# Optimization experiments

Hardware: AMD Instinct MI355X
Metric: run time of the kernel (lower is better)

## Reference

```python
import jax, jax.numpy as jnp
import numpy as np

EMB = 768
HEADS = 12
HEAD_DIM = EMB // HEADS
LN_EPS = 1e-5


def _layernorm(x, g, b):
    mu = jnp.mean(x, axis=-1, keepdims=True)
    var = jnp.mean(jnp.square(x - mu), axis=-1, keepdims=True)
    return (x - mu) * jax.lax.rsqrt(var + LN_EPS) * g + b


def _att_block(x, ln_g, ln_b, w_qkv, b_qkv, w_proj, b_proj):
    # x: [b, n, e]
    B, N, E = x.shape
    h, d = HEADS, HEAD_DIM
    qkv = _layernorm(x, ln_g, ln_b) @ w_qkv.T + b_qkv          # [b, n, 3e]
    # einops 'b n (h d qkv)': last axis factors as (h, d, 3), qkv innermost
    qkv = qkv.reshape(B, N, h, d, 3)
    qkv = jnp.moveaxis(qkv, (4, 2), (0, 2))                    # [3, b, h, n, d]
    q, k, v = qkv[0], qkv[1], qkv[2]
    scale = d ** (-0.5)
    # NOTE: original code DIVIDES by scale (= multiplies by sqrt(d)) -- faithful
    scores = jnp.einsum('bhqd,bhkd->bhqk', q, k) / scale       # [b, h, n, n]
    attn = jax.nn.softmax(scores, axis=-1)
    out = jnp.einsum('bhqk,bhkd->bhqd', attn, v)               # [b, h, n, d]
    out = out.transpose(0, 2, 1, 3).reshape(B, N, E)           # [b, n, e]
    return x + out @ w_proj.T + b_proj


def setup_inputs() -> dict:
    key = jax.random.key(0)
    ks = jax.random.split(key, 8)
    B, N, E = 2, 2048, EMB
    s = E ** (-0.5)
    return {
        'modal1': jax.random.normal(ks[0], (B, N, E), jnp.float32),
        'modal2': jax.random.normal(ks[1], (B, N, E), jnp.float32),
        'ln1_g': jnp.ones((E,), jnp.float32),
        'ln1_b': jnp.zeros((E,), jnp.float32),
        'w_qkv1': jax.random.normal(ks[2], (3 * E, E), jnp.float32) * s,
        'b_qkv1': jnp.zeros((3 * E,), jnp.float32),
        'w_proj1': jax.random.normal(ks[3], (E, E), jnp.float32) * s,
        'b_proj1': jnp.zeros((E,), jnp.float32),
        'ln2_g': jnp.ones((E,), jnp.float32),
        'ln2_b': jnp.zeros((E,), jnp.float32),
        'w_qkv2': jax.random.normal(ks[4], (3 * E, E), jnp.float32) * s,
        'b_qkv2': jnp.zeros((3 * E,), jnp.float32),
        'w_proj2': jax.random.normal(ks[5], (E, E), jnp.float32) * s,
        'b_proj2': jnp.zeros((E,), jnp.float32),
    }


def reference(modal1, modal2, ln1_g, ln1_b, w_qkv1, b_qkv1, w_proj1, b_proj1,
              ln2_g, ln2_b, w_qkv2, b_qkv2, w_proj2, b_proj2):
    out1 = _att_block(modal1, ln1_g, ln1_b, w_qkv1, b_qkv1, w_proj1, b_proj1)
    out2 = _att_block(modal2, ln2_g, ln2_b, w_qkv2, b_qkv2, w_proj2, b_proj2)
    return (out1, out2)
```

## Files before the change

kernel.cpp:

```cpp
#include <hip/hip_runtime.h>
#include <hip/hip_bf16.h>


typedef unsigned short u16;
typedef unsigned int   u32;
typedef __attribute__((ext_vector_type(4)))  float floatx4;
typedef __attribute__((ext_vector_type(16))) float floatx16;
typedef __attribute__((ext_vector_type(8)))  short shortx8;
typedef __attribute__((ext_vector_type(2)))  unsigned int uintx2;

#define EMB   768
#define SEQ   2048
#define NHEAD 12
#define HDIM  64
#define RPM   4096
#define NROW  8192
#define NUNIT 48
#define KTS   4096

__device__ __forceinline__ float bf2f(u16 h) {
  union { u32 u; float f; } v; v.u = ((u32)h) << 16; return v.f;
}
__device__ __forceinline__ u16 f2bf(float f) {
  union { float f; u32 u; } v; v.f = f;
  u32 r = v.u + 0x7fffu + ((v.u >> 16) & 1u);
  return (u16)(r >> 16);
}
__device__ __forceinline__ u32 cvtpk_bf16(float a, float b) {
  u32 r;
  asm("v_cvt_pk_bf16_f32 %0, %1, %2" : "=v"(r) : "v"(a), "v"(b));
  return r;
}
__device__ __forceinline__ void swap_halves(u32 a, u32 b, u32& x, u32& y) {
#if __has_builtin(__builtin_amdgcn_permlane32_swap)
  uintx2 r = __builtin_amdgcn_permlane32_swap(a, b, false, false);
  x = r.x; y = r.y;
#else
  u32 ax = (u32)__shfl_xor((int)a, 32);
  u32 bx = (u32)__shfl_xor((int)b, 32);
  bool h = (threadIdx.x & 32) != 0;
  x = h ? bx : a;
  y = h ? b : ax;
#endif
}

__global__ __launch_bounds__(256) void prep_wq(
    const float* __restrict__ wq1, const float* __restrict__ wq2,
    u16* __restrict__ wh, u16* __restrict__ wl)
{
  int bx = blockIdx.x;
  int modal = bx / 2304, rowp = bx % 2304;
  int typ = rowp / 768, hd = rowp % 768;
  const float* W = (modal ? wq2 : wq1) + (size_t)(hd * 3 + typ) * EMB;
  size_t dst = (size_t)bx * EMB;
  int t = threadIdx.x;
  #pragma unroll
  for (int i = 0; i < 3; ++i) {
    int e = t + i * 256;
    float v = W[e];
    u16 h = f2bf(v);
    wh[dst + e] = h;
    wl[dst + e] = f2bf(v - bf2f(h));
  }
}

__global__ __launch_bounds__(256) void prep_wp(
    const float* __restrict__ wp1, const float* __restrict__ wp2,
    u16* __restrict__ wh)
{
  int bx = blockIdx.x;
  int modal = bx / 768, row = bx % 768;
  const float* W = (modal ? wp2 : wp1) + (size_t)row * EMB;
  size_t dst = (size_t)bx * EMB;
  int t = threadIdx.x;
  #pragma unroll
  for (int i = 0; i < 3; ++i) {
    int e = t + i * 256;
    wh[dst + e] = f2bf(W[e]);
  }
}

__global__ __launch_bounds__(256) void k_ln(
    const float* __restrict__ x1, const float* __restrict__ x2,
    const float* __restrict__ g1, const float* __restrict__ b1,
    const float* __restrict__ g2, const float* __restrict__ b2,
    u16* __restrict__ xn_hi, u16* __restrict__ xn_lo)
{
  int row = blockIdx.x;
  int modal = row >> 12;
  const float* x = modal ? x2 : x1;
  const float* g = modal ? g2 : g1;
  const float* bb = modal ? b2 : b1;
  int r = row & (RPM - 1);
  const float* xr = x + (size_t)r * EMB;
  int t = threadIdx.x;
  float v0 = xr[t], v1 = xr[t + 256], v2 = xr[t + 512];
  float s = v0 + v1 + v2;
  float s2 = v0 * v0 + v1 * v1 + v2 * v2;
  #pragma unroll
  for (int m = 1; m < 64; m <<= 1) { s += __shfl_xor(s, m); s2 += __shfl_xor(s2, m); }
  __shared__ float ls[4], ls2[4];
  int w = t >> 6;
  if ((t & 63) == 0) { ls[w] = s; ls2[w] = s2; }
  __syncthreads();
  s = ls[0] + ls[1] + ls[2] + ls[3];
  s2 = ls2[0] + ls2[1] + ls2[2] + ls2[3];
  float mu = s * (1.0f / EMB);
  float var = s2 * (1.0f / EMB) - mu * mu;
  float rs = rsqrtf(var + 1e-5f);
  size_t base = (size_t)row * EMB;
  float vv[3] = { v0, v1, v2 };
  #pragma unroll
  for (int i = 0; i < 3; ++i) {
    int e = t + i * 256;
    float xn = (vv[i] - mu) * rs * g[e] + bb[e];
    u16 h = f2bf(xn);
    xn_hi[base + e] = h;
    xn_lo[base + e] = f2bf(xn - bf2f(h));
  }
}

__global__ __launch_bounds__(256) void k_qkv(
    const u16* __restrict__ xn_hi, const u16* __restrict__ xn_lo,
    const u16* __restrict__ wqh, const u16* __restrict__ wql,
    const float* __restrict__ bq1, const float* __restrict__ bq2,
    u16* __restrict__ q_hi, u16* __restrict__ q_lo,
    u16* __restrict__ k_hi, u16* __restrict__ k_lo,
    u16* __restrict__ vT)
{
  int mt = blockIdx.x, ntile = blockIdx.y, modal = blockIdx.z;
  const float* BQ = modal ? bq2 : bq1;
  int typ = ntile / 6;
  int hd0 = (ntile % 6) * 128;

  __shared__ __align__(16) u16 As_hi[2][128 * 32], Wh[2][128 * 32],
                               As_lo[2][128 * 32], Wl[2][128 * 32];

  int tid = threadIdx.x, lane = tid & 63, w = tid >> 6;
  int wm = (w >> 1) * 64, wn = (w & 1) * 64;
  int lc = lane & 15, lq = lane >> 4;

  int srow = lane >> 2;
  int schunk = ((lane & 3) ^ (srow & 3)) << 3;

  floatx4 acc[4][4] = {};
  const u16* aH = xn_hi + (size_t)(modal * RPM + mt * 128) * EMB;
  const u16* aL = xn_lo + (size_t)(modal * RPM + mt * 128) * EMB;
  const u16* wH = wqh + (size_t)(modal * 2304 + typ * 768 + hd0) * EMB;
  const u16* wL = wql + (size_t)(modal * 2304 + typ * 768 + hd0) * EMB;

  auto stage = [&](int buf, int k0) {
    if (typ != 2) {
      #pragma unroll
      for (int c = 0; c < 8; ++c) {
        int seg = w * 8 + c;
        int tile = seg >> 3, segin = seg & 7;
        size_t off = (size_t)(segin * 16 + srow) * EMB + k0 + schunk;
        const u16* src; u16* dstb;
        if (tile == 0)      { src = aH + off; dstb = &As_hi[buf][0]; }
        else if (tile == 1) { src = wH + off; dstb = &Wh[buf][0]; }
        else if (tile == 2) { src = aL + off; dstb = &As_lo[buf][0]; }
        else                { src = wL + off; dstb = &Wl[buf][0]; }
        __builtin_amdgcn_global_load_lds(
            (const __attribute__((address_space(1))) unsigned int*)src,
            (__attribute__((address_space(3))) unsigned int*)(dstb + segin * 512), 16, 0, 0);
      }
    } else {
      #pragma unroll
      for (int c = 0; c < 4; ++c) {
        int seg = w * 4 + c;
        int tile = seg >> 3, segin = seg & 7;
        size_t off = (size_t)(segin * 16 + srow) * EMB + k0 + schunk;
        const u16* src; u16* dstb;
        if (tile == 0) { src = aH + off; dstb = &As_hi[buf][0]; }
        else           { src = wH + off; dstb = &Wh[buf][0]; }
        __builtin_amdgcn_global_load_lds(
            (const __attribute__((address_space(1))) unsigned int*)src,
            (__attribute__((address_space(3))) unsigned int*)(dstb + segin * 512), 16, 0, 0);
      }
    }
  };

  stage(0, 0);
  for (int kk = 0; kk < 24; ++kk) {
    int cur = kk & 1;
    bool more = (kk + 1 < 24);
    if (more) stage(cur ^ 1, (kk + 1) * 32);
    if (typ != 2) {
      if (more) asm volatile("s_waitcnt vmcnt(8)" ::: "memory");
      else      asm volatile("s_waitcnt vmcnt(0)" ::: "memory");
    } else {
      if (more) asm volatile("s_waitcnt vmcnt(4)" ::: "memory");
      else      asm volatile("s_waitcnt vmcnt(0)" ::: "memory");
    }
    __builtin_amdgcn_s_barrier();
    __builtin_amdgcn_sched_barrier(0);

    shortx8 ah[4], al[4], whf[4], wlf[4];
    int rsw = lc & 3;
    int ca = (lq ^ rsw) << 3;
    #pragma unroll
    for (int i = 0; i < 4; ++i) {
      int ra = wm + i * 16 + lc, rw = wn + i * 16 + lc;
      ah[i]  = *(const shortx8*)&As_hi[cur][ra * 32 + ca];
      whf[i] = *(const shortx8*)&Wh[cur][rw * 32 + ca];
      if (typ != 2) {
        al[i]  = *(const shortx8*)&As_lo[cur][ra * 32 + ca];
        wlf[i] = *(const shortx8*)&Wl[cur][rw * 32 + ca];
      }
    }
    #pragma unroll
    for (int i = 0; i < 4; ++i)
      #pragma unroll
      for (int jn = 0; jn < 4; ++jn) {
        acc[i][jn] = __builtin_amdgcn_mfma_f32_16x16x32_bf16(ah[i], whf[jn], acc[i][jn], 0, 0, 0);
        if (typ != 2) {
          acc[i][jn] = __builtin_amdgcn_mfma_f32_16x16x32_bf16(al[i], whf[jn], acc[i][jn], 0, 0, 0);
          acc[i][jn] = __builtin_amdgcn_mfma_f32_16x16x32_bf16(ah[i], wlf[jn], acc[i][jn], 0, 0, 0);
        }
      }
    asm volatile("s_waitcnt lgkmcnt(0)" ::: "memory");
    __builtin_amdgcn_s_barrier();
    __builtin_amdgcn_sched_barrier(0);
  }

  #pragma unroll
  for (int i = 0; i < 4; ++i) {
    int mrow0 = mt * 128 + wm + i * 16 + lq * 4;
    #pragma unroll
    for (int jn = 0; jn < 4; ++jn) {
      int colp = hd0 + wn + jn * 16 + lc;
      int h = colp >> 6, d = colp & 63;
      float bias = BQ[colp * 3 + typ];
      #pragma unroll
      for (int r = 0; r < 4; ++r) {
        int mrow = mrow0 + r;
        int b = mrow >> 11, nq = mrow & (SEQ - 1);
        int uu = modal * 24 + b * 12 + h;
        float val = acc[i][jn][r] + bias;
        if (typ == 0) {
          size_t o = ((size_t)uu * SEQ + nq) * HDIM + d;
          u16 hh = f2bf(val); q_hi[o] = hh; q_lo[o] = f2bf(val - bf2f(hh));
        } else if (typ == 1) {
          size_t o = ((size_t)uu * SEQ + nq) * HDIM + d;
          u16 hh = f2bf(val); k_hi[o] = hh; k_lo[o] = f2bf(val - bf2f(hh));
        } else {
          vT[((size_t)uu * HDIM + d) * SEQ + nq] = f2bf(val);
        }
      }
    }
  }
}

__global__ __launch_bounds__(256, 3) void k_attn(
    const u16* __restrict__ q_hi, const u16* __restrict__ q_lo,
    const u16* __restrict__ k_hi, const u16* __restrict__ k_lo,
    const u16* __restrict__ vT, u16* __restrict__ attn_out)
{
  int id = blockIdx.x + (blockIdx.y << 4);
  int xcd = id & 7, j = id >> 3;
  int u = xcd * 6 + (j >> 4);
  int qt = j & 15;

  __shared__ __align__(16) u16 lds[2][3 * KTS];

  int tid = threadIdx.x, lane = tid & 63, w = tid >> 6;
  int col = lane & 31, hi = lane >> 5;
  int swz = (col & 7) << 4;

  shortx8 qh[4], qlo[4];
  {
    size_t qb = ((size_t)u * SEQ + qt * 128 + w * 32 + col) * HDIM + hi * 8;
    #pragma unroll
    for (int s = 0; s < 4; ++s) {
      qh[s]  = *(const shortx8*)(q_hi + qb + s * 16);
      qlo[s] = *(const shortx8*)(q_lo + qb + s * 16);
    }
  }

  int lrow = lane >> 3;
  int lcol = ((lane & 7) ^ lrow) << 3;
  const u16* kh_src = k_hi + (size_t)u * SEQ * HDIM;
  const u16* kl_src = k_lo + (size_t)u * SEQ * HDIM;
  const u16* v_src  = vT  + (size_t)u * HDIM * SEQ;

  auto stage = [&](int buf, int kc) {
    #pragma unroll
    for (int c = 0; c < 6; ++c) {
      int seg = w * 6 + c;
      int tile = seg >> 3, segin = seg & 7;
      u16* dst = &lds[buf][tile * KTS + segin * 512];
      const u16* src;
      if (tile == 0)      src = kh_src + (size_t)(kc + segin * 8 + lrow) * HDIM + lcol;
      else if (tile == 1) src = kl_src + (size_t)(kc + segin * 8 + lrow) * HDIM + lcol;
      else                src = v_src  + (size_t)(segin * 8 + lrow) * SEQ + kc + lcol;
      __builtin_amdgcn_global_load_lds(
          (const __attribute__((address_space(1))) unsigned int*)src,
          (__attribute__((address_space(3))) unsigned int*)dst, 16, 0, 0);
    }
  };

  shortx8 ONES;
  #pragma unroll
  for (int i = 0; i < 8; ++i) ONES[i] = (short)0x3F80;

  floatx16 O0 = {}, O1 = {};
  floatx16 Osum = {};
  float m_r = -1e30f;
  const float Cs = 11.5415603271f;
  const float THR = 8.0f;

  stage(0, 0);
  __syncthreads();

  for (int t = 0; t < SEQ / 64; ++t) {
    int cur = t & 1;
    if (t + 1 < SEQ / 64) stage(cur ^ 1, (t + 1) * 64);

    const char* Kh = (const char*)&lds[cur][0];
    const char* Kl = (const char*)&lds[cur][KTS];
    const char* Vt = (const char*)&lds[cur][2 * KTS];

    floatx16 S0 = {}, S1 = {};
    __builtin_amdgcn_s_setprio(1);
    #pragma unroll
    for (int s = 0; s < 4; ++s) {
      int cb = (s * 32 + hi * 16) ^ swz;
      shortx8 kf0 = *(const shortx8*)(Kh + col * 128 + cb);
      shortx8 kl0 = *(const shortx8*)(Kl + col * 128 + cb);
      shortx8 kf1 = *(const shortx8*)(Kh + (32 + col) * 128 + cb);
      shortx8 kl1 = *(const shortx8*)(Kl + (32 + col) * 128 + cb);
      S0 = __builtin_amdgcn_mfma_f32_32x32x16_bf16(kf0, qh[s],  S0, 0, 0, 0);
      S1 = __builtin_amdgcn_mfma_f32_32x32x16_bf16(kf1, qh[s],  S1, 0, 0, 0);
      S0 = __builtin_amdgcn_mfma_f32_32x32x16_bf16(kf0, qlo[s], S0, 0, 0, 0);
      S1 = __builtin_amdgcn_mfma_f32_32x32x16_bf16(kf1, qlo[s], S1, 0, 0, 0);
      S0 = __builtin_amdgcn_mfma_f32_32x32x16_bf16(kl0, qh[s],  S0, 0, 0, 0);
      S1 = __builtin_amdgcn_mfma_f32_32x32x16_bf16(kl1, qh[s],  S1, 0, 0, 0);
    }
    __builtin_amdgcn_s_setprio(0);

    float pm[16];
    #pragma unroll
    for (int r = 0; r < 16; ++r) pm[r] = fmaxf(S0[r], S1[r]);
    float g0 = fmaxf(fmaxf(pm[0],  pm[1]),  pm[2]);
    float g1 = fmaxf(fmaxf(pm[3],  pm[4]),  pm[5]);
    float g2 = fmaxf(fmaxf(pm[6],  pm[7]),  pm[8]);
    float g3 = fmaxf(fmaxf(pm[9],  pm[10]), pm[11]);
    float g4 = fmaxf(fmaxf(pm[12], pm[13]), pm[14]);
    float mx = fmaxf(fmaxf(fmaxf(g0, g1), g2), fmaxf(fmaxf(g3, g4), pm[15])) * Cs;
    mx = fmaxf(mx, __shfl_xor(mx, 32));

    if (!__all(mx <= m_r + THR)) {
      float mn = fmaxf(m_r, mx);
      float alpha = __builtin_amdgcn_exp2f(m_r - mn);
      m_r = mn;
      #pragma unroll
      for (int r = 0; r < 16; ++r) {
        int qsrc = (r & 3) + 8 * (r >> 2) + 4 * hi;
        union { float f; int i; } a; a.f = alpha;
        a.i = __builtin_amdgcn_ds_bpermute(qsrc << 2, a.i);
        O0[r] *= a.f; O1[r] *= a.f; Osum[r] *= a.f;
      }
    }

    #pragma unroll
    for (int ks = 0; ks < 4; ++ks) {
      const int h2 = ks & 1;
      float ee[8];
      #pragma unroll
      for (int i = 0; i < 8; ++i) {
        float sv = (ks < 2) ? S0[h2 * 8 + i] : S1[h2 * 8 + i];
        ee[i] = __builtin_amdgcn_exp2f(fmaf(Cs, sv, -m_r));
      }
      u32 A = cvtpk_bf16(ee[0], ee[1]);
      u32 B = cvtpk_bf16(ee[2], ee[3]);
      u32 C = cvtpk_bf16(ee[4], ee[5]);
      u32 D = cvtpk_bf16(ee[6], ee[7]);
      u32 w0, w1, w2, w3;
      swap_halves(A, C, w0, w2);
      swap_halves(B, D, w1, w3);
      union { u32 uu[4]; shortx8 ss; } pk_;
      pk_.uu[0] = w0; pk_.uu[1] = w1; pk_.uu[2] = w2; pk_.uu[3] = w3;
      int cb = (ks * 32 + hi * 16) ^ swz;
      shortx8 v0 = *(const shortx8*)(Vt + col * 128 + cb);
      shortx8 v1 = *(const shortx8*)(Vt + (32 + col) * 128 + cb);
      O0   = __builtin_amdgcn_mfma_f32_32x32x16_bf16(pk_.ss, v0,   O0,   0, 0, 0);
      O1   = __builtin_amdgcn_mfma_f32_32x32x16_bf16(pk_.ss, v1,   O1,   0, 0, 0);
      Osum = __builtin_amdgcn_mfma_f32_32x32x16_bf16(pk_.ss, ONES, Osum, 0, 0, 0);
    }

    __syncthreads();
  }

  int modal = u / 24, b = (u / 12) & 1, h = u % 12;
  size_t obase = ((size_t)(modal * RPM + b * SEQ + qt * 128 + w * 32)) * EMB + h * 64 + col;
  #pragma unroll
  for (int r = 0; r < 16; ++r) {
    int ql_ = (r & 3) + 8 * (r >> 2) + 4 * hi;
    float rl = __builtin_amdgcn_rcpf(Osum[r]);
    size_t ob = obase + (size_t)ql_ * EMB;
    attn_out[ob]      = f2bf(O0[r] * rl);
    attn_out[ob + 32] = f2bf(O1[r] * rl);
  }
}

__global__ __launch_bounds__(256) void k_proj(
    const u16* __restrict__ ao, const u16* __restrict__ wph,
    const float* __restrict__ x1, const float* __restrict__ x2,
    const float* __restrict__ bp1, const float* __restrict__ bp2,
    float* __restrict__ out)
{
  int mt = blockIdx.x, ntile = blockIdx.y, modal = blockIdx.z;
  const float* BP = modal ? bp2 : bp1;
  const float* x  = modal ? x2 : x1;

  __shared__ __align__(16) u16 As[2][64 * 32], Ws[2][128 * 32];
  int tid = threadIdx.x, lane = tid & 63, w = tid >> 6;
  int wm = (w >> 1) * 32, wn = (w & 1) * 64;
  int lc = lane & 15, lq = lane >> 4;

  int srow = lane >> 2;
  int schunk = ((lane & 3) ^ (srow & 3)) << 3;

  floatx4 acc[2][4] = {};
  const u16* aP = ao  + (size_t)(modal * RPM + mt * 64) * EMB;
  const u16* wP = wph + (size_t)(modal * 768 + ntile * 128) * EMB;

  auto stage = [&](int buf, int k0) {
    #pragma unroll
    for (int c = 0; c < 3; ++c) {
      int seg = w * 3 + c;
      const u16* src; u16* dst;
      if (seg < 4) {
        src = aP + (size_t)(seg * 16 + srow) * EMB + k0 + schunk;
        dst = &As[buf][0] + seg * 512;
      } else {
        int s2 = seg - 4;
        src = wP + (size_t)(s2 * 16 + srow) * EMB + k0 + schunk;
        dst = &Ws[buf][0] + s2 * 512;
      }
      __builtin_amdgcn_global_load_lds(
          (const __attribute__((address_space(1))) unsigned int*)src,
          (__attribute__((address_space(3))) unsigned int*)dst, 16, 0, 0);
    }
  };

  stage(0, 0);
  for (int kk = 0; kk < 24; ++kk) {
    int cur = kk & 1;
    bool more = (kk + 1 < 24);
    if (more) stage(cur ^ 1, (kk + 1) * 32);
    if (more) asm volatile("s_waitcnt vmcnt(3)" ::: "memory");
    else      asm volatile("s_waitcnt vmcnt(0)" ::: "memory");
    __builtin_amdgcn_s_barrier();
    __builtin_amdgcn_sched_barrier(0);

    int ca = (lq ^ (lc & 3)) << 3;
    shortx8 af[2], wf[4];
    #pragma unroll
    for (int i = 0; i < 2; ++i) af[i] = *(const shortx8*)&As[cur][(wm + i * 16 + lc) * 32 + ca];
    #pragma unroll
    for (int i = 0; i < 4; ++i) wf[i] = *(const shortx8*)&Ws[cur][(wn + i * 16 + lc) * 32 + ca];
    #pragma unroll
    for (int i = 0; i < 2; ++i)
      #pragma unroll
      for (int jn = 0; jn < 4; ++jn)
        acc[i][jn] = __builtin_amdgcn_mfma_f32_16x16x32_bf16(af[i], wf[jn], acc[i][jn], 0, 0, 0);
    asm volatile("s_waitcnt lgkmcnt(0)" ::: "memory");
    __builtin_amdgcn_s_barrier();
    __builtin_amdgcn_sched_barrier(0);
  }

  #pragma unroll
  for (int i = 0; i < 2; ++i) {
    int mrow0 = mt * 64 + wm + i * 16 + lq * 4;
    #pragma unroll
    for (int jn = 0; jn < 4; ++jn) {
      int col = ntile * 128 + wn + jn * 16 + lc;
      float bias = BP[col];
      #pragma unroll
      for (int r = 0; r < 4; ++r) {
        int mrow = mrow0 + r;
        float val = acc[i][jn][r] + bias + x[(size_t)mrow * EMB + col];
        out[((size_t)(modal * RPM + mrow)) * EMB + col] = val;
      }
    }
  }
}

extern "C" void kernel_launch(void* const* d_in, const int* in_sizes, int n_in,
                              void* d_out, int out_size, void* d_ws, size_t ws_size,
                              hipStream_t stream) {
  const float* modal1 = (const float*)d_in[0];
  const float* modal2 = (const float*)d_in[1];
  const float* ln1_g  = (const float*)d_in[2];
  const float* ln1_b  = (const float*)d_in[3];
  const float* w_qkv1 = (const float*)d_in[4];
  const float* b_qkv1 = (const float*)d_in[5];
  const float* w_proj1= (const float*)d_in[6];
  const float* b_proj1= (const float*)d_in[7];
  const float* ln2_g  = (const float*)d_in[8];
  const float* ln2_b  = (const float*)d_in[9];
  const float* w_qkv2 = (const float*)d_in[10];
  const float* b_qkv2 = (const float*)d_in[11];
  const float* w_proj2= (const float*)d_in[12];
  const float* b_proj2= (const float*)d_in[13];
  float* out = (float*)d_out;

  const size_t BUFE = (size_t)NROW * EMB;
  const size_t WQE  = (size_t)2 * 2304 * EMB;
  u16* xn_hi = (u16*)d_ws;
  u16* xn_lo = xn_hi + BUFE;
  u16* q_hi  = xn_lo + BUFE;
  u16* q_lo  = q_hi + BUFE;
  u16* k_hi  = q_lo + BUFE;
  u16* k_lo  = k_hi + BUFE;
  u16* vT    = k_lo + BUFE;
  u16* wq_h  = vT + BUFE;
  u16* wq_l  = wq_h + WQE;
  u16* attn  = xn_hi;
  u16* wp_h  = q_lo;

  prep_wq<<<4608, 256, 0, stream>>>(w_qkv1, w_qkv2, wq_h, wq_l);
  k_ln<<<NROW, 256, 0, stream>>>(modal1, modal2, ln1_g, ln1_b, ln2_g, ln2_b, xn_hi, xn_lo);
  dim3 g2(32, 18, 2);
  k_qkv<<<g2, 256, 0, stream>>>(xn_hi, xn_lo, wq_h, wq_l, b_qkv1, b_qkv2,
                                q_hi, q_lo, k_hi, k_lo, vT);
  dim3 g3(16, 48);
  k_attn<<<g3, 256, 0, stream>>>(q_hi, q_lo, k_hi, k_lo, vT, attn);
  prep_wp<<<1536, 256, 0, stream>>>(w_proj1, w_proj2, wp_h);
  dim3 g4(64, 6, 2);
  k_proj<<<g4, 256, 0, stream>>>(attn, wp_h, modal1, modal2, b_proj1, b_proj2, out);
}
```

Baseline: 387.2 us.

## Replace ones-MFMA row sum with VALU reduction and merge LN with weight prep

The attention kernel no longer runs a third MFMA against an all-ones matrix to build the softmax denominator. Each lane now sums its exponentials in registers, the two half-waves are combined with a shuffle at the end, and the reciprocal is redistributed with bpermute. This cuts matrix-core work in the PV loop by a third at the cost of extra VALU adds. The kernel also computes all exponentials and packs them before the PV MFMAs, under raised priority. Separately, the weight-prep and layernorm kernels are merged into one launch to save a kernel boundary.

```diff
diff --git a/kernel.cpp b/kernel.cpp
--- a/kernel.cpp
+++ b/kernel.cpp
@@ -44,23 +44,61 @@
 #endif
 }
 
-__global__ __launch_bounds__(256) void prep_wq(
+__global__ __launch_bounds__(256) void k_pre(
     const float* __restrict__ wq1, const float* __restrict__ wq2,
-    u16* __restrict__ wh, u16* __restrict__ wl)
+    u16* __restrict__ wh, u16* __restrict__ wl,
+    const float* __restrict__ x1, const float* __restrict__ x2,
+    const float* __restrict__ g1, const float* __restrict__ b1,
+    const float* __restrict__ g2, const float* __restrict__ b2,
+    u16* __restrict__ xn_hi, u16* __restrict__ xn_lo)
 {
   int bx = blockIdx.x;
-  int modal = bx / 2304, rowp = bx % 2304;
-  int typ = rowp / 768, hd = rowp % 768;
-  const float* W = (modal ? wq2 : wq1) + (size_t)(hd * 3 + typ) * EMB;
-  size_t dst = (size_t)bx * EMB;
   int t = threadIdx.x;
-  #pragma unroll
-  for (int i = 0; i < 3; ++i) {
-    int e = t + i * 256;
-    float v = W[e];
-    u16 h = f2bf(v);
-    wh[dst + e] = h;
-    wl[dst + e] = f2bf(v - bf2f(h));
+  if (bx < 4608) {
+    int modal = bx / 2304, rowp = bx % 2304;
+    int typ = rowp / 768, hd = rowp % 768;
+    const float* W = (modal ? wq2 : wq1) + (size_t)(hd * 3 + typ) * EMB;
+    size_t dst = (size_t)bx * EMB;
+    #pragma unroll
+    for (int i = 0; i < 3; ++i) {
+      int e = t + i * 256;
+      float v = W[e];
+      u16 h = f2bf(v);
+      wh[dst + e] = h;
+      wl[dst + e] = f2bf(v - bf2f(h));
+    }
+  } else {
+    int row = bx - 4608;
+    int modal = row >> 12;
+    const float* x = modal ? x2 : x1;
+    const float* g = modal ? g2 : g1;
+    const float* bb = modal ? b2 : b1;
+    int r = row & (RPM - 1);
+    const float* xr = x + (size_t)r * EMB;
+    float v0 = xr[t], v1 = xr[t + 256], v2 = xr[t + 512];
+    float s = v0 + v1 + v2;
+    float s2 = v0 * v0 + v1 * v1 + v2 * v2;
+    #pragma unroll
+    for (int m = 1; m < 64; m <<= 1) { s += __shfl_xor(s, m); s2 += __shfl_xor(s2, m); }
+    __shared__ float ls[4], ls2[4];
+    int w = t >> 6;
+    if ((t & 63) == 0) { ls[w] = s; ls2[w] = s2; }
+    __syncthreads();
+    s = ls[0] + ls[1] + ls[2] + ls[3];
+    s2 = ls2[0] + ls2[1] + ls2[2] + ls2[3];
+    float mu = s * (1.0f / EMB);
+    float var = s2 * (1.0f / EMB) - mu * mu;
+    float rs = rsqrtf(var + 1e-5f);
+    size_t base = (size_t)row * EMB;
+    float vv[3] = { v0, v1, v2 };
+    #pragma unroll
+    for (int i = 0; i < 3; ++i) {
+      int e = t + i * 256;
+      float xn = (vv[i] - mu) * rs * g[e] + bb[e];
+      u16 h = f2bf(xn);
+      xn_hi[base + e] = h;
+      xn_lo[base + e] = f2bf(xn - bf2f(h));
+    }
   }
 }
 
@@ -77,46 +115,6 @@
   for (int i = 0; i < 3; ++i) {
     int e = t + i * 256;
     wh[dst + e] = f2bf(W[e]);
-  }
-}
-
-__global__ __launch_bounds__(256) void k_ln(
-    const float* __restrict__ x1, const float* __restrict__ x2,
-    const float* __restrict__ g1, const float* __restrict__ b1,
-    const float* __restrict__ g2, const float* __restrict__ b2,
-    u16* __restrict__ xn_hi, u16* __restrict__ xn_lo)
-{
-  int row = blockIdx.x;
-  int modal = row >> 12;
-  const float* x = modal ? x2 : x1;
-  const float* g = modal ? g2 : g1;
-  const float* bb = modal ? b2 : b1;
-  int r = row & (RPM - 1);
-  const float* xr = x + (size_t)r * EMB;
-  int t = threadIdx.x;
-  float v0 = xr[t], v1 = xr[t + 256], v2 = xr[t + 512];
-  float s = v0 + v1 + v2;
-  float s2 = v0 * v0 + v1 * v1 + v2 * v2;
-  #pragma unroll
-  for (int m = 1; m < 64; m <<= 1) { s += __shfl_xor(s, m); s2 += __shfl_xor(s2, m); }
-  __shared__ float ls[4], ls2[4];
-  int w = t >> 6;
-  if ((t & 63) == 0) { ls[w] = s; ls2[w] = s2; }
-  __syncthreads();
-  s = ls[0] + ls[1] + ls[2] + ls[3];
-  s2 = ls2[0] + ls2[1] + ls2[2] + ls2[3];
-  float mu = s * (1.0f / EMB);
-  float var = s2 * (1.0f / EMB) - mu * mu;
-  float rs = rsqrtf(var + 1e-5f);
-  size_t base = (size_t)row * EMB;
-  float vv[3] = { v0, v1, v2 };
-  #pragma unroll
-  for (int i = 0; i < 3; ++i) {
-    int e = t + i * 256;
-    float xn = (vv[i] - mu) * rs * g[e] + bb[e];
-    u16 h = f2bf(xn);
-    xn_hi[base + e] = h;
-    xn_lo[base + e] = f2bf(xn - bf2f(h));
   }
 }
 
@@ -300,13 +298,8 @@
     }
   };
 
-  shortx8 ONES;
-  #pragma unroll
-  for (int i = 0; i < 8; ++i) ONES[i] = (short)0x3F80;
-
   floatx16 O0 = {}, O1 = {};
-  floatx16 Osum = {};
-  float m_r = -1e30f;
+  float m_r = -1e30f, lsum = 0.0f;
   const float Cs = 11.5415603271f;
   const float THR = 8.0f;
 
@@ -339,68 +332,88 @@
     }
     __builtin_amdgcn_s_setprio(0);
 
-    float pm[16];
-    #pragma unroll
-    for (int r = 0; r < 16; ++r) pm[r] = fmaxf(S0[r], S1[r]);
-    float g0 = fmaxf(fmaxf(pm[0],  pm[1]),  pm[2]);
-    float g1 = fmaxf(fmaxf(pm[3],  pm[4]),  pm[5]);
-    float g2 = fmaxf(fmaxf(pm[6],  pm[7]),  pm[8]);
-    float g3 = fmaxf(fmaxf(pm[9],  pm[10]), pm[11]);
-    float g4 = fmaxf(fmaxf(pm[12], pm[13]), pm[14]);
-    float mx = fmaxf(fmaxf(fmaxf(g0, g1), g2), fmaxf(fmaxf(g3, g4), pm[15])) * Cs;
+    float tm[16];
+    #pragma unroll
+    for (int r = 0; r < 16; ++r) tm[r] = fmaxf(S0[r], S1[r]);
+    #pragma unroll
+    for (int st = 8; st >= 1; st >>= 1)
+      #pragma unroll
+      for (int i = 0; i < st; ++i) tm[i] = fmaxf(tm[i], tm[i + st]);
+    float mx = tm[0] * Cs;
     mx = fmaxf(mx, __shfl_xor(mx, 32));
 
     if (!__all(mx <= m_r + THR)) {
       float mn = fmaxf(m_r, mx);
       float alpha = __builtin_amdgcn_exp2f(m_r - mn);
       m_r = mn;
+      lsum *= alpha;
       #pragma unroll
       for (int r = 0; r < 16; ++r) {
         int qsrc = (r & 3) + 8 * (r >> 2) + 4 * hi;
         union { float f; int i; } a; a.f = alpha;
         a.i = __builtin_amdgcn_ds_bpermute(qsrc << 2, a.i);
-        O0[r] *= a.f; O1[r] *= a.f; Osum[r] *= a.f;
-      }
-    }
-
+        O0[r] *= a.f; O1[r] *= a.f;
+      }
+    }
+
+    #pragma unroll
+    for (int r = 0; r < 16; ++r) {
+      S0[r] = __builtin_amdgcn_exp2f(fmaf(Cs, S0[r], -m_r));
+      S1[r] = __builtin_amdgcn_exp2f(fmaf(Cs, S1[r], -m_r));
+    }
+    #pragma unroll
+    for (int r = 0; r < 16; ++r) tm[r] = S0[r] + S1[r];
+    #pragma unroll
+    for (int st = 8; st >= 1; st >>= 1)
+      #pragma unroll
+      for (int i = 0; i < st; ++i) tm[i] += tm[i + st];
+    lsum += tm[0];
+
+    shortx8 pf[4];
+    #pragma unroll
+    for (int kt = 0; kt < 2; ++kt)
+      #pragma unroll
+      for (int h2 = 0; h2 < 2; ++h2) {
+        floatx16 Sv = kt ? S1 : S0;
+        int b0 = h2 * 8;
+        u32 A = cvtpk_bf16(Sv[b0 + 0], Sv[b0 + 1]);
+        u32 B = cvtpk_bf16(Sv[b0 + 2], Sv[b0 + 3]);
+        u32 C = cvtpk_bf16(Sv[b0 + 4], Sv[b0 + 5]);
+        u32 D = cvtpk_bf16(Sv[b0 + 6], Sv[b0 + 7]);
+        u32 w0, w1, w2, w3;
+        swap_halves(A, C, w0, w2);
+        swap_halves(B, D, w1, w3);
+        union { u32 uu[4]; shortx8 ss; } pk_;
+        pk_.uu[0] = w0; pk_.uu[1] = w1; pk_.uu[2] = w2; pk_.uu[3] = w3;
+        pf[kt * 2 + h2] = pk_.ss;
+      }
+
+    __builtin_amdgcn_s_setprio(1);
     #pragma unroll
     for (int ks = 0; ks < 4; ++ks) {
-      const int h2 = ks & 1;
-      float ee[8];
-      #pragma unroll
-      for (int i = 0; i < 8; ++i) {
-        float sv = (ks < 2) ? S0[h2 * 8 + i] : S1[h2 * 8 + i];
-        ee[i] = __builtin_amdgcn_exp2f(fmaf(Cs, sv, -m_r));
-      }
-      u32 A = cvtpk_bf16(ee[0], ee[1]);
-      u32 B = cvtpk_bf16(ee[2], ee[3]);
-      u32 C = cvtpk_bf16(ee[4], ee[5]);
-      u32 D = cvtpk_bf16(ee[6], ee[7]);
-      u32 w0, w1, w2, w3;
-      swap_halves(A, C, w0, w2);
-      swap_halves(B, D, w1, w3);
-      union { u32 uu[4]; shortx8 ss; } pk_;
-      pk_.uu[0] = w0; pk_.uu[1] = w1; pk_.uu[2] = w2; pk_.uu[3] = w3;
       int cb = (ks * 32 + hi * 16) ^ swz;
       shortx8 v0 = *(const shortx8*)(Vt + col * 128 + cb);
       shortx8 v1 = *(const shortx8*)(Vt + (32 + col) * 128 + cb);
-      O0   = __builtin_amdgcn_mfma_f32_32x32x16_bf16(pk_.ss, v0,   O0,   0, 0, 0);
-      O1   = __builtin_amdgcn_mfma_f32_32x32x16_bf16(pk_.ss, v1,   O1,   0, 0, 0);
-      Osum = __builtin_amdgcn_mfma_f32_32x32x16_bf16(pk_.ss, ONES, Osum, 0, 0, 0);
-    }
+      O0 = __builtin_amdgcn_mfma_f32_32x32x16_bf16(pf[ks], v0, O0, 0, 0, 0);
+      O1 = __builtin_amdgcn_mfma_f32_32x32x16_bf16(pf[ks], v1, O1, 0, 0, 0);
+    }
+    __builtin_amdgcn_s_setprio(0);
 
     __syncthreads();
   }
 
+  float lt = lsum + __shfl_xor(lsum, 32);
+  float rl = __builtin_amdgcn_rcpf(lt);
   int modal = u / 24, b = (u / 12) & 1, h = u % 12;
   size_t obase = ((size_t)(modal * RPM + b * SEQ + qt * 128 + w * 32)) * EMB + h * 64 + col;
   #pragma unroll
   for (int r = 0; r < 16; ++r) {
     int ql_ = (r & 3) + 8 * (r >> 2) + 4 * hi;
-    float rl = __builtin_amdgcn_rcpf(Osum[r]);
+    union { float f; int i; } a; a.f = rl;
+    a.i = __builtin_amdgcn_ds_bpermute(ql_ << 2, a.i);
     size_t ob = obase + (size_t)ql_ * EMB;
-    attn_out[ob]      = f2bf(O0[r] * rl);
-    attn_out[ob + 32] = f2bf(O1[r] * rl);
+    attn_out[ob]      = f2bf(O0[r] * a.f);
+    attn_out[ob + 32] = f2bf(O1[r] * a.f);
   }
 }
 
@@ -521,8 +534,9 @@
   u16* attn  = xn_hi;
   u16* wp_h  = q_lo;
 
-  prep_wq<<<4608, 256, 0, stream>>>(w_qkv1, w_qkv2, wq_h, wq_l);
-  k_ln<<<NROW, 256, 0, stream>>>(modal1, modal2, ln1_g, ln1_b, ln2_g, ln2_b, xn_hi, xn_lo);
+  k_pre<<<4608 + NROW, 256, 0, stream>>>(w_qkv1, w_qkv2, wq_h, wq_l,
+                                         modal1, modal2, ln1_g, ln1_b, ln2_g, ln2_b,
+                                         xn_hi, xn_lo);
   dim3 g2(32, 18, 2);
   k_qkv<<<g2, 256, 0, stream>>>(xn_hi, xn_lo, wq_h, wq_l, b_qkv1, b_qkv2,
                                 q_hi, q_lo, k_hi, k_lo, vT);
```

After: 349.7 us. 1.11x faster.
